# Kernel optimization log

Hardware: AMD Instinct MI355X
Metric: run time of the kernel (lower is better)

The kernel has to match this reference:

```python
import jax, jax.numpy as jnp
import numpy as np

K = 501   # box-filter length (conv kernel height)
P = 250   # reflect padding on each side of the time axis


def setup_inputs() -> dict:
    key = jax.random.key(0)
    k1, k2 = jax.random.split(key)
    pred = jax.random.normal(k1, (8, 16384, 128), dtype=jnp.float32)  # [B, T, C]
    # Conv2d default bias init: U(-b, b) with b = 1/sqrt(fan_in) = 1/sqrt(501)
    b = 1.0 / np.sqrt(K)
    bias = jax.random.uniform(k2, (1,), dtype=jnp.float32, minval=-b, maxval=b)
    return {"pred": pred, "bias": bias}


def reference(pred, bias):
    # Reflect-pad the time axis, then compute the 501-wide moving sum via a
    # prefix-sum (O(N) instead of O(N*K) dense conv) — same math as the
    # all-ones Conv2d kernel with reflect padding.
    x = jnp.pad(pred, ((0, 0), (P, P), (0, 0)), mode="reflect")  # [B, T+2P, C]
    c = jnp.cumsum(x, axis=1)
    c = jnp.concatenate([jnp.zeros_like(c[:, :1, :]), c], axis=1)  # [B, T+2P+1, C]
    win_sum = c[:, K:, :] - c[:, :-K, :]                            # [B, T, C]
    smoothed = (win_sum + bias[0]) / K  # conv output (ones weights + bias) / kernel_size
    return jnp.maximum(pred, smoothed)
```

## Files before the change

kernel.cpp:

```cpp
#include <hip/hip_runtime.h>


constexpr int B    = 8;
constexpr int T    = 16384;
constexpr int C    = 128;
constexpr int K    = 501;
constexpr int Pp   = 250;
constexpr int CHN  = 16;
constexpr int NCG  = C / CHN;
constexpr int NSEG = 8;
constexpr int SEGR = T / NSEG;
constexpr int RING = 1024;
constexpr int CHK  = 64;
constexpr int NC   = (SEGR + 512) / CHK;
constexpr int PRO  = 12;

__device__ __forceinline__ int ridx(int j) {
    j = (j < 0) ? -j : j;
    return (j >= T) ? (2 * T - 2 - j) : j;
}

__device__ __forceinline__ void dma16(const float* g, float* l) {
    __builtin_amdgcn_global_load_lds(
        (const __attribute__((address_space(1))) void*)g,
        (__attribute__((address_space(3))) void*)l, 16, 0, 0);
}
__device__ __forceinline__ void dma4(const float* g, float* l) {
    __builtin_amdgcn_global_load_lds(
        (const __attribute__((address_space(1))) void*)g,
        (__attribute__((address_space(3))) void*)l, 4, 0, 0);
}

__global__ __launch_bounds__(64) void smoother_kernel(
    const float* __restrict__ pred, const float* __restrict__ bias,
    float* __restrict__ out) {
    __shared__ float ring[RING * CHN];

    const int b   = blockIdx.x & 7;
    const int cg  = (blockIdx.x >> 3) & 7;
    const int seg = blockIdx.x >> 6;
    const int g0  = seg * SEGR;
    const int jstart = g0 - 256;

    const int lane = threadIdx.x & 63;
    const int q    = lane >> 4;
    const int ch   = lane & 15;

    const float* pb = pred + (size_t)b * T * C;
    float*       ob = out  + (size_t)b * T * C + cg * CHN + ch;

    const float rk  = 1.0f / (float)K;
    const float brk = bias[0] * rk;

    auto stage = [&](int m) {
        const int j0  = jstart + m * CHK;
        const int ph0 = (m * CHK) & (RING - 1);
        if (j0 >= 0 && j0 + CHK - 1 < T) {
            #pragma unroll
            for (int i = 0; i < 4; ++i) {
                const float* g = pb + (size_t)(j0 + 16 * i + (lane >> 2)) * C
                               + cg * CHN + (lane & 3) * 4;
                dma16(g, &ring[(size_t)(ph0 + 16 * i) * CHN]);
            }
        } else {
            #pragma unroll
            for (int i = 0; i < 16; ++i) {
                const int jr = ridx(j0 + 4 * i + (lane >> 4));
                const float* g = pb + (size_t)jr * C + cg * CHN + (lane & 15);
                dma4(g, &ring[(size_t)(ph0 + 4 * i) * CHN]);
            }
        }
    };

    for (int m = 0; m < PRO; ++m) stage(m);

    float acc = 0.0f;
    #pragma unroll 5
    for (int i = 0; i < 125; ++i)
        acc += ring[(size_t)(6 + 4 * i + q) * CHN + ch];
    float a2 = acc + __shfl_xor(acc, 16);
    float S  = a2 + __shfl_xor(a2, 32);
    S += ring[(size_t)506 * CHN + ch];

    int rn = 507 + q;
    int ro = 6   + q;
    int rc = 256 + q;
    int my_t = g0 + q;

    for (int k = 0; k < SEGR / CHK; ++k) {
        #pragma unroll 4
        for (int i = 0; i < CHK / 4; ++i) {
            const float vn = ring[(size_t)rn * CHN + ch];
            const float vo = ring[(size_t)ro * CHN + ch];
            const float vc = ring[(size_t)rc * CHN + ch];
            const float d  = vn - vo;
            float x = d;
            const float u1 = __shfl_up(x, 16); if (lane >= 16) x += u1;
            const float u2 = __shfl_up(x, 32); if (lane >= 32) x += u2;
            const float tot = __shfl(x, 48 + ch);
            const float sm  = S + (x - d);
            const float o   = fmaxf(vc, fmaf(sm, rk, brk));
            __builtin_nontemporal_store(o, &ob[(size_t)my_t * C]);
            S += tot;
            rn = (rn + 4) & (RING - 1);
            ro = (ro + 4) & (RING - 1);
            rc = (rc + 4) & (RING - 1);
            my_t += 4;
        }
        if (PRO + k < NC) stage(PRO + k);
    }
}

extern "C" void kernel_launch(void* const* d_in, const int* in_sizes, int n_in,
                              void* d_out, int out_size, void* d_ws, size_t ws_size,
                              hipStream_t stream) {
    const float* pred = (const float*)d_in[0];
    const float* bias = (const float*)d_in[1];
    float*       out  = (float*)d_out;

    const int blocks = B * NCG * NSEG;
    smoother_kernel<<<blocks, 64, 0, stream>>>(pred, bias, out);
}
```

Measured before the change: 145.1 us.

## Replace LDS ring DMA staging with direct global loads and more segments

```diff
diff --git a/kernel.cpp b/kernel.cpp
--- a/kernel.cpp
+++ b/kernel.cpp
@@ -5,109 +5,89 @@
 constexpr int T    = 16384;
 constexpr int C    = 128;
 constexpr int K    = 501;
-constexpr int Pp   = 250;
 constexpr int CHN  = 16;
 constexpr int NCG  = C / CHN;
-constexpr int NSEG = 8;
+constexpr int NSEG = 32;
 constexpr int SEGR = T / NSEG;
-constexpr int RING = 1024;
-constexpr int CHK  = 64;
-constexpr int NC   = (SEGR + 512) / CHK;
-constexpr int PRO  = 12;
 
 __device__ __forceinline__ int ridx(int j) {
     j = (j < 0) ? -j : j;
     return (j >= T) ? (2 * T - 2 - j) : j;
 }
 
-__device__ __forceinline__ void dma16(const float* g, float* l) {
-    __builtin_amdgcn_global_load_lds(
-        (const __attribute__((address_space(1))) void*)g,
-        (__attribute__((address_space(3))) void*)l, 16, 0, 0);
-}
-__device__ __forceinline__ void dma4(const float* g, float* l) {
-    __builtin_amdgcn_global_load_lds(
-        (const __attribute__((address_space(1))) void*)g,
-        (__attribute__((address_space(3))) void*)l, 4, 0, 0);
-}
-
-__global__ __launch_bounds__(64) void smoother_kernel(
+__global__ __launch_bounds__(64, 4) void smoother_kernel(
     const float* __restrict__ pred, const float* __restrict__ bias,
     float* __restrict__ out) {
-    __shared__ float ring[RING * CHN];
-
     const int b   = blockIdx.x & 7;
     const int cg  = (blockIdx.x >> 3) & 7;
     const int seg = blockIdx.x >> 6;
     const int g0  = seg * SEGR;
-    const int jstart = g0 - 256;
 
     const int lane = threadIdx.x & 63;
     const int q    = lane >> 4;
     const int ch   = lane & 15;
 
-    const float* pb = pred + (size_t)b * T * C;
+    const float* pb = pred + (size_t)b * T * C + cg * CHN + ch;
     float*       ob = out  + (size_t)b * T * C + cg * CHN + ch;
 
     const float rk  = 1.0f / (float)K;
     const float brk = bias[0] * rk;
 
-    auto stage = [&](int m) {
-        const int j0  = jstart + m * CHK;
-        const int ph0 = (m * CHK) & (RING - 1);
-        if (j0 >= 0 && j0 + CHK - 1 < T) {
-            #pragma unroll
-            for (int i = 0; i < 4; ++i) {
-                const float* g = pb + (size_t)(j0 + 16 * i + (lane >> 2)) * C
-                               + cg * CHN + (lane & 3) * 4;
-                dma16(g, &ring[(size_t)(ph0 + 16 * i) * CHN]);
-            }
-        } else {
-            #pragma unroll
-            for (int i = 0; i < 16; ++i) {
-                const int jr = ridx(j0 + 4 * i + (lane >> 4));
-                const float* g = pb + (size_t)jr * C + cg * CHN + (lane & 15);
-                dma4(g, &ring[(size_t)(ph0 + 4 * i) * CHN]);
-            }
-        }
-    };
-
-    for (int m = 0; m < PRO; ++m) stage(m);
+    const bool interior = (g0 >= 251) && (g0 + SEGR + 251 <= T);
 
     float acc = 0.0f;
-    #pragma unroll 5
-    for (int i = 0; i < 125; ++i)
-        acc += ring[(size_t)(6 + 4 * i + q) * CHN + ch];
+    if (interior) {
+        #pragma unroll 5
+        for (int i = 0; i < 125; ++i)
+            acc += pb[(g0 - 250 + 4 * i + q) * C];
+    } else {
+        #pragma unroll 5
+        for (int i = 0; i < 125; ++i)
+            acc += pb[ridx(g0 - 250 + 4 * i + q) * C];
+    }
     float a2 = acc + __shfl_xor(acc, 16);
     float S  = a2 + __shfl_xor(a2, 32);
-    S += ring[(size_t)506 * CHN + ch];
+    S += pb[(interior ? (g0 + 250) : ridx(g0 + 250)) * C];
 
-    int rn = 507 + q;
-    int ro = 6   + q;
-    int rc = 256 + q;
-    int my_t = g0 + q;
+    int tn = g0 + 251 + q;
+    int to = g0 - 250 + q;
+    int tc = g0 + q;
+    const int srcl = 48 + ch;
 
-    for (int k = 0; k < SEGR / CHK; ++k) {
-        #pragma unroll 4
-        for (int i = 0; i < CHK / 4; ++i) {
-            const float vn = ring[(size_t)rn * CHN + ch];
-            const float vo = ring[(size_t)ro * CHN + ch];
-            const float vc = ring[(size_t)rc * CHN + ch];
+    if (interior) {
+        #pragma unroll 8
+        for (int i = 0; i < SEGR / 4; ++i) {
+            const float vn = pb[tn * C];
+            const float vo = pb[to * C];
+            const float vc = pb[tc * C];
             const float d  = vn - vo;
             float x = d;
             const float u1 = __shfl_up(x, 16); if (lane >= 16) x += u1;
             const float u2 = __shfl_up(x, 32); if (lane >= 32) x += u2;
-            const float tot = __shfl(x, 48 + ch);
+            const float tot = __shfl(x, srcl);
             const float sm  = S + (x - d);
             const float o   = fmaxf(vc, fmaf(sm, rk, brk));
-            __builtin_nontemporal_store(o, &ob[(size_t)my_t * C]);
+            __builtin_nontemporal_store(o, &ob[tc * C]);
             S += tot;
-            rn = (rn + 4) & (RING - 1);
-            ro = (ro + 4) & (RING - 1);
-            rc = (rc + 4) & (RING - 1);
-            my_t += 4;
+            tn += 4; to += 4; tc += 4;
         }
-        if (PRO + k < NC) stage(PRO + k);
+    } else {
+        #pragma unroll 4
+        for (int i = 0; i < SEGR / 4; ++i) {
+            const float vn = pb[ridx(tn) * C];
+            const float vo = pb[ridx(to) * C];
+            const float vc = pb[tc * C];
+            const float d  = vn - vo;
+            float x = d;
+            const float u1 = __shfl_up(x, 16); if (lane >= 16) x += u1;
+            const float u2 = __shfl_up(x, 32); if (lane >= 32) x += u2;
+            const float tot = __shfl(x, srcl);
+            const float sm  = S + (x - d);
+            const float o   = fmaxf(vc, fmaf(sm, rk, brk));
+            __builtin_nontemporal_store(o, &ob[tc * C]);
+            S += tot;
+            tn += 4; to += 4; tc += 4;
+        }
     }
 }
 
```

Measured after the change: 146.6 us. Within noise of the previous version (+1.0%).
